# Optimization experiments

Hardware: AMD Instinct MI355X
Metric: run time of the kernel (lower is better)

The kernel has to match this reference:

```python
import jax, jax.numpy as jnp
from jax import lax
import numpy as np

L = 4
KH, KW = 3, 3


def setup_inputs() -> dict:
    key = jax.random.key(0)
    k1, k2, k3, k4 = jax.random.split(key, 4)
    B, H, W, C = 32, 512, 512, 3
    inputs = jax.random.normal(k1, (B, H, W, C), dtype=jnp.float32)
    # posterior_loc ~ 'random_normal' initializer (stddev 0.05 in keras)
    posterior_loc = 0.05 * jax.random.normal(k2, (KH, KW, C, 1), dtype=jnp.float32)
    # posterior_scale initialized to constant -5.0 (small perturbation for non-degeneracy)
    posterior_scale = jnp.full((KH, KW, C, 1), -5.0, dtype=jnp.float32) + 0.1 * jax.random.normal(k3, (KH, KW, C, 1), dtype=jnp.float32)
    # reparameterization noise, one independent sample per pyramid level
    eps = jax.random.normal(k4, (L, KH, KW, C, 1), dtype=jnp.float32)
    return {"inputs": inputs, "posterior_loc": posterior_loc, "posterior_scale": posterior_scale, "eps": eps}


def _center_mask(dtype):
    # zero at the kernel center, one elsewhere (scatter of sampled values into non-center taps)
    m = np.ones((KH, KW, 1, 1), dtype=np.float32)
    m[KH // 2, KW // 2, 0, 0] = 0.0
    return jnp.asarray(m, dtype=dtype)


def _depthwise(x, kernel_hwc1):
    # x: [B,h,w,C], kernel_hwc1: [KH,KW,C,1] (TF depthwise layout) -> HWIO [KH,KW,1,C]
    C = x.shape[-1]
    k = jnp.transpose(kernel_hwc1, (0, 1, 3, 2))
    return lax.conv_general_dilated(
        x, k, window_strides=(1, 1), padding="SAME",
        dimension_numbers=("NHWC", "HWIO", "NHWC"), feature_group_count=C)


def reference(inputs, posterior_loc, posterior_scale, eps):
    B, H, W, C = inputs.shape
    sigma = jax.nn.softplus(posterior_scale)  # posterior stddev
    mask = _center_mask(inputs.dtype)
    total_error = jnp.zeros((B, H, W), dtype=inputs.dtype)
    for l in range(1, L + 1):
        factor = 2 ** (l - 1)
        th, tw = H // factor, W // factor
        ds = jax.image.resize(inputs, (B, th, tw, C), method="bilinear", antialias=True)
        # sampled Bayesian kernel: center tap zeroed, then normalized per channel
        v = posterior_loc + sigma * eps[l - 1]
        kern = v * mask
        kern = kern / (jnp.sum(kern, axis=(0, 1), keepdims=True) + 1e-7)
        r_hat = _depthwise(ds, kern)
        err = ds - r_hat
        up = jax.image.resize(err, (B, H, W, C), method="bilinear", antialias=False)
        total_error = total_error + jnp.sum(up, axis=-1)
    recon = jnp.mean(jnp.sum(jnp.square(total_error), axis=(1, 2)))
    # KL(N(mu, sigma) || N(0,1)), summed; added once per conv call -> L times
    kl = jnp.sum(-jnp.log(sigma) + 0.5 * (jnp.square(sigma) + jnp.square(posterior_loc)) - 0.5)
    return recon + L * kl
```

## Files before the change

kernel.cpp:

```cpp
#include <hip/hip_runtime.h>
#include <hip/hip_fp16.h>
#include <math.h>

#define BB 32
#define HH 512
#define WW 512
#define CC 3
#define LL 4

typedef _Float16 h2_t __attribute__((ext_vector_type(2)));

static __device__ __forceinline__ float softplusf_(float x) {
    if (x > 20.f) return x;
    return log1pf(expf(x));
}
static __device__ __forceinline__ int iclamp_(int v, int lo, int hi) {
    return v < lo ? lo : (v > hi ? hi : v);
}

__global__ void prep_kernel(const float* __restrict__ loc, const float* __restrict__ scale,
                            const float* __restrict__ eps, float* __restrict__ knorm,
                            double* __restrict__ kl_out) {
    int tid = threadIdx.x;
    float klv = 0.f;
    if (tid < 27) {
        float s = softplusf_(scale[tid]);
        float m = loc[tid];
        klv = -logf(s) + 0.5f * (s * s + m * m) - 0.5f;
    }
    #pragma unroll
    for (int off = 32; off; off >>= 1) klv += __shfl_down(klv, off);
    if (tid == 0) *kl_out = (double)klv;
    if (tid < 12) {
        int l = tid / 3;
        int c = tid - l * 3;
        float v[9];
        float sum = 0.f;
        #pragma unroll
        for (int t = 0; t < 9; ++t) {
            int idx = t * 3 + c;
            float s = softplusf_(scale[idx]);
            float val = loc[idx] + s * eps[l * 27 + idx];
            if (t == 4) val = 0.f;
            v[t] = val;
            sum += val;
        }
        float denom = sum + 1e-7f;
        #pragma unroll
        for (int t = 0; t < 9; ++t)
            knorm[l * 27 + t * 3 + c] = v[t] / denom;
    }
}

#define PSH 544
#define RESC 1.1428571428571428f

__global__ void hpass_kernel(const float* __restrict__ x, __half* __restrict__ xh2,
                             __half* __restrict__ xh4, __half* __restrict__ xh8) {
    __shared__ __align__(16) __half planes[4 * 3 * PSH];
    const int tid = threadIdx.x;
    const int lane = tid & 63;
    const int wv = tid >> 6;
    const int bh = blockIdx.x * 4 + wv;
    __half* pl = planes + wv * (3 * PSH);

    const float4* src = (const float4*)(x + bh * (WW * CC));
    #pragma unroll
    for (int s = 0; s < 6; ++s) {
        int i = lane + (s << 6);
        float4 v = src[i];
        int g = i << 2;
        int j = g / 3;
        int c = g - j * 3;
        float e[4] = {v.x, v.y, v.z, v.w};
        #pragma unroll
        for (int u = 0; u < 4; ++u) {
            pl[c * PSH + 17 + j] = __float2half_rn(e[u]);
            ++c;
            if (c == 3) { c = 0; ++j; }
        }
    }
    {
        int t = lane;
        if (t < 96) {
            int pp = t >> 5, k = t & 31;
            int hi = (k < 17) ? k : (512 + k);
            pl[pp * PSH + hi] = __float2half_rn(0.f);
        }
        t = lane + 64;
        if (t < 96) {
            int pp = t >> 5, k = t & 31;
            int hi = (k < 17) ? k : (512 + k);
            pl[pp * PSH + hi] = __float2half_rn(0.f);
        }
    }
    asm volatile("s_waitcnt lgkmcnt(0)" ::: "memory");

    if (xh2) {
        const h2_t P0 = {(_Float16)0.125f, (_Float16)0.375f};
        const h2_t P1 = {(_Float16)0.375f, (_Float16)0.125f};
        __half* o2 = xh2 + bh * 768;
        #pragma unroll
        for (int s = 0; s < 4; ++s) {
            int ow = lane + (s << 6);
            float res[3];
            #pragma unroll
            for (int c = 0; c < 3; ++c) {
                const __half* p = pl + c * PSH;
                int hb2 = 2 * lane + 128 * s + 16;
                h2_t v0 = *(const h2_t*)&p[hb2];
                h2_t v1 = *(const h2_t*)&p[hb2 + 2];
                float a = __builtin_amdgcn_fdot2(v0, P0, 0.f, false);
                a = __builtin_amdgcn_fdot2(v1, P1, a, false);
                res[c] = a;
            }
            if (s == 0 && lane == 0) { res[0] *= RESC; res[1] *= RESC; res[2] *= RESC; }
            if (s == 3 && lane == 63) { res[0] *= RESC; res[1] *= RESC; res[2] *= RESC; }
            o2[ow * 3 + 0] = __float2half_rn(res[0]);
            o2[ow * 3 + 1] = __float2half_rn(res[1]);
            o2[ow * 3 + 2] = __float2half_rn(res[2]);
        }
    }
    if (xh4) {
        const h2_t P0 = {(_Float16)0.f,      (_Float16)0.03125f};
        const h2_t P1 = {(_Float16)0.09375f, (_Float16)0.15625f};
        const h2_t P2 = {(_Float16)0.21875f, (_Float16)0.21875f};
        const h2_t P3 = {(_Float16)0.15625f, (_Float16)0.09375f};
        const h2_t P4 = {(_Float16)0.03125f, (_Float16)0.f};
        __half* o4 = xh4 + bh * 384;
        #pragma unroll
        for (int s = 0; s < 2; ++s) {
            int ow = lane + (s << 6);
            float res[3];
            #pragma unroll
            for (int c = 0; c < 3; ++c) {
                const __half* p = pl + c * PSH;
                int hb2 = 4 * lane + 256 * s + 14;
                float a = __builtin_amdgcn_fdot2(*(const h2_t*)&p[hb2], P0, 0.f, false);
                a = __builtin_amdgcn_fdot2(*(const h2_t*)&p[hb2 + 2], P1, a, false);
                a = __builtin_amdgcn_fdot2(*(const h2_t*)&p[hb2 + 4], P2, a, false);
                a = __builtin_amdgcn_fdot2(*(const h2_t*)&p[hb2 + 6], P3, a, false);
                a = __builtin_amdgcn_fdot2(*(const h2_t*)&p[hb2 + 8], P4, a, false);
                res[c] = a;
            }
            if (s == 0 && lane == 0) { res[0] *= RESC; res[1] *= RESC; res[2] *= RESC; }
            if (s == 1 && lane == 63) { res[0] *= RESC; res[1] *= RESC; res[2] *= RESC; }
            o4[ow * 3 + 0] = __float2half_rn(res[0]);
            o4[ow * 3 + 1] = __float2half_rn(res[1]);
            o4[ow * 3 + 2] = __float2half_rn(res[2]);
        }
    }
    if (xh8) {
        const h2_t Q0 = {(_Float16)0.f,         (_Float16)0.0078125f};
        const h2_t Q1 = {(_Float16)0.0234375f,  (_Float16)0.0390625f};
        const h2_t Q2 = {(_Float16)0.0546875f,  (_Float16)0.0703125f};
        const h2_t Q3 = {(_Float16)0.0859375f,  (_Float16)0.1015625f};
        const h2_t Q4 = {(_Float16)0.1171875f,  (_Float16)0.1171875f};
        const h2_t Q5 = {(_Float16)0.1015625f,  (_Float16)0.0859375f};
        const h2_t Q6 = {(_Float16)0.0703125f,  (_Float16)0.0546875f};
        const h2_t Q7 = {(_Float16)0.0390625f,  (_Float16)0.0234375f};
        const h2_t Q8 = {(_Float16)0.0078125f,  (_Float16)0.f};
        __half* o8 = xh8 + bh * 192;
        int ow = lane;
        float res[3];
        #pragma unroll
        for (int c = 0; c < 3; ++c) {
            const __half* p = pl + c * PSH;
            int hb2 = 8 * lane + 12;
            float a = __builtin_amdgcn_fdot2(*(const h2_t*)&p[hb2], Q0, 0.f, false);
            a = __builtin_amdgcn_fdot2(*(const h2_t*)&p[hb2 + 2], Q1, a, false);
            a = __builtin_amdgcn_fdot2(*(const h2_t*)&p[hb2 + 4], Q2, a, false);
            a = __builtin_amdgcn_fdot2(*(const h2_t*)&p[hb2 + 6], Q3, a, false);
            a = __builtin_amdgcn_fdot2(*(const h2_t*)&p[hb2 + 8], Q4, a, false);
            a = __builtin_amdgcn_fdot2(*(const h2_t*)&p[hb2 + 10], Q5, a, false);
            a = __builtin_amdgcn_fdot2(*(const h2_t*)&p[hb2 + 12], Q6, a, false);
            a = __builtin_amdgcn_fdot2(*(const h2_t*)&p[hb2 + 14], Q7, a, false);
            a = __builtin_amdgcn_fdot2(*(const h2_t*)&p[hb2 + 16], Q8, a, false);
            res[c] = a;
        }
        if (lane == 0) { res[0] *= RESC; res[1] *= RESC; res[2] *= RESC; }
        if (lane == 63) { res[0] *= RESC; res[1] *= RESC; res[2] *= RESC; }
        o8[ow * 3 + 0] = __float2half_rn(res[0]);
        o8[ow * 3 + 1] = __float2half_rn(res[1]);
        o8[ow * 3 + 2] = __float2half_rn(res[2]);
    }
}

template <int F, int THB>
static __device__ __forceinline__ void level_body(const __half* __restrict__ xh,
                                                  const float* __restrict__ knorm_all, int lvl,
                                                  float* __restrict__ es, int bx, int by, int b,
                                                  char* smem_raw) {
    constexpr int TH = HH / F, TW = WW / F, TW3 = TW * 3, TAPS = 2 * F;
    constexpr int RS = (THB + 3) * F;
    constexpr int DR = THB + 2;
    __half* stg = (__half*)smem_raw;
    float* dst = (float*)(smem_raw + RS * 108 * 2);
    float* wvv = dst + DR * 108;
    float* kn = wvv + DR * TAPS;
    int owb = bx * 32, ohb = by * THB;
    int tid = threadIdx.x;
    if (tid < 27) kn[tid] = knorm_all[lvl * 27 + tid];
    if (tid >= 32 && tid < 32 + DR) {
        int r = tid - 32;
        int oh = ohb - 1 + r;
        if (oh < 0 || oh >= TH) {
            #pragma unroll
            for (int k = 0; k < TAPS; ++k) wvv[r * TAPS + k] = 0.f;
        } else {
            float sfh = (oh + 0.5f) * F - 0.5f;
            int j0 = oh * F - F / 2;
            float tmp[TAPS]; float s = 0.f;
            #pragma unroll
            for (int k = 0; k < TAPS; ++k) {
                int j = j0 + k;
                float w = (j >= 0 && j < HH) ? (1.f - fabsf(j - sfh) * (1.0f / F)) : 0.f;
                tmp[k] = w; s += w;
            }
            float inv = 1.f / s;
            #pragma unroll
            for (int k = 0; k < TAPS; ++k) wvv[r * TAPS + k] = tmp[k] * inv;
        }
    }
    int jmin = (ohb - 1) * F - F / 2;
    int cb = owb * 3 - 4;
    bool fast = (cb >= 0) && (cb + 108 <= TW3);
    const __half* xb = xh + b * (HH * TW3);
    for (int i = tid; i < RS * 27; i += 256) {
        int r = i / 27;
        int c4 = (i - r * 27) * 4;
        int jh = iclamp_(jmin + r, 0, HH - 1);
        const __half* rp = xb + jh * TW3;
        if (fast) {
            *(ushort4*)&stg[r * 108 + c4] = *(const ushort4*)(rp + cb + c4);
        } else {
            #pragma unroll
            for (int u = 0; u < 4; ++u) {
                int col = iclamp_(cb + c4 + u, 0, TW3 - 1);
                stg[r * 108 + c4 + u] = rp[col];
            }
        }
    }
    __syncthreads();
    for (int i = tid; i < DR * 27; i += 256) {
        int r = i / 27;
        int c4 = (i - r * 27) * 4;
        int gc = cb + c4;
        float v0 = 0, v1 = 0, v2 = 0, v3 = 0;
        if ((unsigned)gc < (unsigned)TW3) {
            const __half* sp = &stg[r * F * 108 + c4];
            const float* wr = &wvv[r * TAPS];
            #pragma unroll
            for (int k = 0; k < TAPS; ++k) {
                float wk = wr[k];
                const __half2* h2 = (const __half2*)(sp + k * 108);
                float2 f0 = __half22float2(h2[0]);
                float2 f1 = __half22float2(h2[1]);
                v0 += wk * f0.x; v1 += wk * f0.y;
                v2 += wk * f1.x; v3 += wk * f1.y;
            }
        }
        float4 q; q.x = v0; q.y = v1; q.z = v2; q.w = v3;
        *(float4*)&dst[r * 108 + c4] = q;
    }
    __syncthreads();
    for (int i = tid; i < THB * 32; i += 256) {
        int wl = i & 31, hl = i >> 5;
        int base = hl * 108 + wl * 3 + 1;
        float e = 0.f;
        #pragma unroll
        for (int c = 0; c < 3; ++c) {
            float conv = 0.f;
            #pragma unroll
            for (int dh = 0; dh < 3; ++dh)
                #pragma unroll
                for (int dw = 0; dw < 3; ++dw)
                    conv += kn[(dh * 3 + dw) * 3 + c] * dst[base + dh * 108 + dw * 3 + c];
            e += dst[base + 108 + 3 + c] - conv;
        }
        es[b * (TH * TW) + (ohb + hl) * TW + owb + wl] = e;
    }
}

__global__ void levels_kernel(const __half* __restrict__ xh2, const __half* __restrict__ xh4,
                              const __half* __restrict__ xh8, const float* __restrict__ knorm,
                              float* __restrict__ es2, float* __restrict__ es3,
                              float* __restrict__ es4, int block_base) {
    __shared__ __align__(16) char smem[16896];
    int vb = blockIdx.x + block_base;
    if (vb < 4096) {
        level_body<2, 16>(xh2, knorm, 1, es2, vb & 7, (vb >> 3) & 15, vb >> 7, smem);
    } else if (vb < 6144) {
        int l = vb - 4096;
        level_body<4, 8>(xh4, knorm, 2, es3, l & 3, (l >> 2) & 15, l >> 6, smem);
    } else {
        int l = vb - 6144;
        level_body<8, 4>(xh8, knorm, 3, es4, l & 1, (l >> 1) & 15, l >> 5, smem);
    }
}

#define FPS 35
#define FPC (34 * FPS)
__global__ void __launch_bounds__(256, 8)
fused_kernel(const float* __restrict__ x, const float* __restrict__ knorm,
             const float* __restrict__ es2, const float* __restrict__ es3,
             const float* __restrict__ es4, double* __restrict__ partials) {
    __shared__ __align__(16) float planes[3 * FPC];
    __shared__ float e2t[18 * 19];
    __shared__ float e3t[10 * 11];
    __shared__ float e4t[6 * 7];
    __shared__ float kn[27];
    __shared__ float smf[4];
    int b = blockIdx.z;
    int hb = blockIdx.y * 32, wb = blockIdx.x * 32;
    int tid = threadIdx.x;
    if (tid < 27) kn[tid] = knorm[tid];
    const float* xb = x + b * (HH * WW * CC);
    int cb = wb * 3 - 4;
    bool fastc = (cb >= 0) && (cb + 108 <= WW * CC);
    for (int i = tid; i < 918; i += 256) {
        int r = i / 27;
        int f0 = (i - r * 27) * 4;
        int gh = hb - 1 + r;
        bool ghv = (unsigned)gh < (unsigned)HH;
        float vv[4] = {0.f, 0.f, 0.f, 0.f};
        if (ghv) {
            const float* rp = xb + gh * (WW * CC);
            if (fastc) {
                float4 v = *(const float4*)(rp + cb + f0);
                vv[0] = v.x; vv[1] = v.y; vv[2] = v.z; vv[3] = v.w;
            } else {
                int g0 = cb + f0;
                #pragma unroll
                for (int u = 0; u < 4; ++u)
                    vv[u] = ((unsigned)(g0 + u) < (unsigned)(WW * CC)) ? rp[g0 + u] : 0.f;
            }
        }
        #pragma unroll
        for (int u = 0; u < 4; ++u) {
            int f = f0 + u;
            if (f >= 1 && f <= 102) {
                int lc = (f - 1) / 3;
                int ch = (f - 1) - lc * 3;
                planes[ch * FPC + r * FPS + lc] = vv[u];
            }
        }
    }
    {
        const float* e2b = es2 + b * (256 * 256);
        int h0 = hb / 2 - 1, w0 = wb / 2 - 1;
        for (int i = tid; i < 18 * 32; i += 256) {
            int r = i >> 5, c = i & 31;
            if (c < 18) {
                int gh = iclamp_(h0 + r, 0, 255);
                int gw = iclamp_(w0 + c, 0, 255);
                e2t[r * 19 + c] = e2b[gh * 256 + gw];
            }
        }
        const float* e3b = es3 + b * (128 * 128);
        int h03 = hb / 4 - 1, w03 = wb / 4 - 1;
        if (tid < 160) {
            int r = tid >> 4, c = tid & 15;
            if (c < 10) {
                int gh = iclamp_(h03 + r, 0, 127);
                int gw = iclamp_(w03 + c, 0, 127);
                e3t[r * 11 + c] = e3b[gh * 128 + gw];
            }
        }
        const float* e4b = es4 + b * (64 * 64);
        int h04 = hb / 8 - 1, w04 = wb / 8 - 1;
        if (tid < 48) {
            int r = tid >> 3, c = tid & 7;
            if (c < 6) {
                int gh = iclamp_(h04 + r, 0, 63);
                int gw = iclamp_(w04 + c, 0, 63);
                e4t[r * 7 + c] = e4b[gh * 64 + gw];
            }
        }
    }
    __syncthreads();

    int q = tid >> 3;
    int a = tid & 7;
    float cv0 = 0, cv1 = 0, cv2 = 0, cv3 = 0;
    float ce0 = 0, ce1 = 0, ce2 = 0, ce3 = 0;
    #pragma unroll
    for (int c = 0; c < 3; ++c) {
        const float* P = planes + c * FPC;
        #pragma unroll
        for (int dh = 0; dh < 3; ++dh) {
            const float* r0 = P + (q + dh) * FPS + 4 * a;
            float w0 = r0[0], w1 = r0[1], w2 = r0[2], w3 = r0[3], w4 = r0[4], w5 = r0[5];
            float ka = kn[dh * 9 + c], kb = kn[dh * 9 + 3 + c], kc = kn[dh * 9 + 6 + c];
            cv0 += ka * w0 + kb * w1 + kc * w2;
            cv1 += ka * w1 + kb * w2 + kc * w3;
            cv2 += ka * w2 + kb * w3 + kc * w4;
            cv3 += ka * w3 + kb * w4 + kc * w5;
            if (dh == 1) { ce0 += w1; ce1 += w2; ce2 += w3; ce3 += w4; }
        }
    }
    float e[4] = {ce0 - cv0, ce1 - cv1, ce2 - cv2, ce3 - cv3};

    int n2 = q & 1;   float fh2 = n2 ? 0.25f : 0.75f;               int rh2 = (q >> 1) + n2;
    int n4 = q & 3;   float fh4 = ((n4 + 2) & 3) * 0.25f + 0.125f;  int rh4 = (q >> 2) + (n4 < 2 ? 0 : 1);
    int n8 = q & 7;   float fh8 = ((n8 + 4) & 7) * 0.125f + 0.0625f; int rh8 = (q >> 3) + (n8 < 4 ? 0 : 1);
    {
        const float* r0 = &e2t[rh2 * 19 + 2 * a];
        const float* r1 = r0 + 19;
        float t0 = r0[0], t1 = r0[1], t2 = r0[2], t3 = r0[3];
        float b0 = r1[0], b1 = r1[1], b2 = r1[2], b3 = r1[3];
        float top, bot;
        top = t0 + 0.75f * (t1 - t0); bot = b0 + 0.75f * (b1 - b0); e[0] += top + fh2 * (bot - top);
        top = t1 + 0.25f * (t2 - t1); bot = b1 + 0.25f * (b2 - b1); e[1] += top + fh2 * (bot - top);
        top = t1 + 0.75f * (t2 - t1); bot = b1 + 0.75f * (b2 - b1); e[2] += top + fh2 * (bot - top);
        top = t2 + 0.25f * (t3 - t2); bot = b2 + 0.25f * (b3 - b2); e[3] += top + fh2 * (bot - top);
    }
    {
        const float* r0 = &e3t[rh4 * 11 + a];
        const float* r1 = r0 + 11;
        float t0 = r0[0], t1 = r0[1], t2 = r0[2];
        float b0 = r1[0], b1 = r1[1], b2 = r1[2];
        float top, bot;
        top = t0 + 0.625f * (t1 - t0); bot = b0 + 0.625f * (b1 - b0); e[0] += top + fh4 * (bot - top);
        top = t0 + 0.875f * (t1 - t0); bot = b0 + 0.875f * (b1 - b0); e[1] += top + fh4 * (bot - top);
        top = t1 + 0.125f * (t2 - t1); bot = b1 + 0.125f * (b2 - b1); e[2] += top + fh4 * (bot - top);
        top = t1 + 0.375f * (t2 - t1); bot = b1 + 0.375f * (b2 - b1); e[3] += top + fh4 * (bot - top);
    }
    {
        int rw8 = (a >> 1) + (a & 1);
        const float* r0 = &e4t[rh8 * 7 + rw8];
        const float* r1 = r0 + 7;
        float t0 = r0[0], t1 = r0[1];
        float b0 = r1[0], b1 = r1[1];
        float fwb = (a & 1) ? 0.0625f : 0.5625f;
        #pragma unroll
        for (int p = 0; p < 4; ++p) {
            float fw = fwb + 0.125f * p;
            float top = t0 + fw * (t1 - t0);
            float bot = b0 + fw * (b1 - b0);
            e[p] += top + fh8 * (bot - top);
        }
    }
    float acc = e[0] * e[0] + e[1] * e[1] + e[2] * e[2] + e[3] * e[3];
    #pragma unroll
    for (int off = 32; off; off >>= 1) acc += __shfl_down(acc, off);
    if ((tid & 63) == 0) smf[tid >> 6] = acc;
    __syncthreads();
    if (tid == 0) {
        double s = (double)smf[0] + (double)smf[1] + (double)smf[2] + (double)smf[3];
        partials[(b * 16 + blockIdx.y) * 16 + blockIdx.x] = s;
    }
}

__global__ void final_kernel(const double* __restrict__ partials, int n,
                             const double* __restrict__ kl, float* __restrict__ out) {
    __shared__ double sm[1024];
    double acc = 0.0;
    for (int i = threadIdx.x; i < n; i += 1024) acc += partials[i];
    sm[threadIdx.x] = acc;
    __syncthreads();
    for (int s = 512; s > 0; s >>= 1) {
        if (threadIdx.x < (unsigned)s) sm[threadIdx.x] += sm[threadIdx.x + s];
        __syncthreads();
    }
    if (threadIdx.x == 0) out[0] = (float)(sm[0] / (double)BB + (double)LL * kl[0]);
}

extern "C" void kernel_launch(void* const* d_in, const int* in_sizes, int n_in,
                              void* d_out, int out_size, void* d_ws, size_t ws_size,
                              hipStream_t stream) {
    const float* x = (const float*)d_in[0];
    const float* loc = (const float*)d_in[1];
    const float* scale = (const float*)d_in[2];
    const float* eps = (const float*)d_in[3];
    float* out = (float*)d_out;

    char* ws = (char*)d_ws;
    float* knorm = (float*)(ws + 0);
    double* kl = (double*)(ws + 512);
    double* partials = (double*)(ws + 1024);
    float* es4 = (float*)(ws + 131072);
    float* es3 = (float*)(ws + 655360);
    float* es2 = (float*)(ws + 2752512);
    (void)in_sizes; (void)n_in; (void)out_size;

    prep_kernel<<<1, 64, 0, stream>>>(loc, scale, eps, knorm, kl);

    const size_t SINGLE_NEED = 55181312ull;
    if (ws_size >= SINGLE_NEED) {
        __half* xh2 = (__half*)(ws + 11141120);
        __half* xh4 = (__half*)(ws + 36306944);
        __half* xh8 = (__half*)(ws + 48889856);
        hpass_kernel<<<BB * HH / 4, 256, 0, stream>>>(x, xh2, xh4, xh8);
        levels_kernel<<<7168, 256, 0, stream>>>(xh2, xh4, xh8, knorm, es2, es3, es4, 0);
    } else {
        __half* xh4 = (__half*)(ws + 11141120);
        __half* xh8 = (__half*)(ws + 23724032);
        __half* xh2 = (__half*)(ws + 11141120);
        hpass_kernel<<<BB * HH / 4, 256, 0, stream>>>(x, nullptr, xh4, xh8);
        levels_kernel<<<3072, 256, 0, stream>>>(nullptr, xh4, xh8, knorm, es2, es3, es4, 4096);
        hpass_kernel<<<BB * HH / 4, 256, 0, stream>>>(x, xh2, nullptr, nullptr);
        levels_kernel<<<4096, 256, 0, stream>>>(xh2, nullptr, nullptr, knorm, es2, es3, es4, 0);
    }

    fused_kernel<<<dim3(16, 16, BB), 256, 0, stream>>>(x, knorm, es2, es3, es4, partials);
    final_kernel<<<1, 1024, 0, stream>>>(partials, 8192, kl, out);
}
```

Before: 106.1 us.

## Keep interleaved channel layout in shared tile and use vectorized LDS reads

The fused kernel's input tile is now stored in shared memory in its original interleaved NHWC order, written as float4, instead of being scattered into three per-channel planes. The stencil reads 20 floats per row with five float4 loads and skips the zero centre tap explicitly. The aim is to cut the scalar scatter stores and per-element index math during staging and the many scalar LDS reads in the compute loop. In exchange it uses more registers per thread, lowers the launch-bounds occupancy hint from 8 to 6, and the strided float4 LDS reads may cause bank conflicts.

```diff
diff --git a/kernel.cpp b/kernel.cpp
--- a/kernel.cpp
+++ b/kernel.cpp
@@ -299,13 +299,12 @@
     }
 }
 
-#define FPS 35
-#define FPC (34 * FPS)
-__global__ void __launch_bounds__(256, 8)
+#define FXS 116
+__global__ void __launch_bounds__(256, 6)
 fused_kernel(const float* __restrict__ x, const float* __restrict__ knorm,
              const float* __restrict__ es2, const float* __restrict__ es3,
              const float* __restrict__ es4, double* __restrict__ partials) {
-    __shared__ __align__(16) float planes[3 * FPC];
+    __shared__ __align__(16) float xt[34 * FXS];
     __shared__ float e2t[18 * 19];
     __shared__ float e3t[10 * 11];
     __shared__ float e4t[6 * 7];
@@ -316,35 +315,29 @@
     int tid = threadIdx.x;
     if (tid < 27) kn[tid] = knorm[tid];
     const float* xb = x + b * (HH * WW * CC);
-    int cb = wb * 3 - 4;
-    bool fastc = (cb >= 0) && (cb + 108 <= WW * CC);
-    for (int i = tid; i < 918; i += 256) {
-        int r = i / 27;
-        int f0 = (i - r * 27) * 4;
+    const int cb2 = wb * 3 - 4;
+    for (int i = tid; i < 34 * 29; i += 256) {
+        int r = i / 29;
+        int k = i - r * 29;
         int gh = hb - 1 + r;
         bool ghv = (unsigned)gh < (unsigned)HH;
-        float vv[4] = {0.f, 0.f, 0.f, 0.f};
+        int g0 = cb2 + 4 * k;
+        float4 v = {0.f, 0.f, 0.f, 0.f};
         if (ghv) {
             const float* rp = xb + gh * (WW * CC);
-            if (fastc) {
-                float4 v = *(const float4*)(rp + cb + f0);
-                vv[0] = v.x; vv[1] = v.y; vv[2] = v.z; vv[3] = v.w;
+            if (g0 >= 0 && g0 + 4 <= WW * CC) {
+                v = *(const float4*)(rp + g0);
             } else {
-                int g0 = cb + f0;
+                float vv[4];
                 #pragma unroll
-                for (int u = 0; u < 4; ++u)
-                    vv[u] = ((unsigned)(g0 + u) < (unsigned)(WW * CC)) ? rp[g0 + u] : 0.f;
-            }
-        }
-        #pragma unroll
-        for (int u = 0; u < 4; ++u) {
-            int f = f0 + u;
-            if (f >= 1 && f <= 102) {
-                int lc = (f - 1) / 3;
-                int ch = (f - 1) - lc * 3;
-                planes[ch * FPC + r * FPS + lc] = vv[u];
-            }
-        }
+                for (int u = 0; u < 4; ++u) {
+                    int g = g0 + u;
+                    vv[u] = ((unsigned)g < (unsigned)(WW * CC)) ? rp[g] : 0.f;
+                }
+                v.x = vv[0]; v.y = vv[1]; v.z = vv[2]; v.w = vv[3];
+            }
+        }
+        *(float4*)&xt[r * FXS + 4 * k] = v;
     }
     {
         const float* e2b = es2 + b * (256 * 256);
@@ -385,18 +378,31 @@
     float cv0 = 0, cv1 = 0, cv2 = 0, cv3 = 0;
     float ce0 = 0, ce1 = 0, ce2 = 0, ce3 = 0;
     #pragma unroll
-    for (int c = 0; c < 3; ++c) {
-        const float* P = planes + c * FPC;
-        #pragma unroll
-        for (int dh = 0; dh < 3; ++dh) {
-            const float* r0 = P + (q + dh) * FPS + 4 * a;
-            float w0 = r0[0], w1 = r0[1], w2 = r0[2], w3 = r0[3], w4 = r0[4], w5 = r0[5];
-            float ka = kn[dh * 9 + c], kb = kn[dh * 9 + 3 + c], kc = kn[dh * 9 + 6 + c];
-            cv0 += ka * w0 + kb * w1 + kc * w2;
-            cv1 += ka * w1 + kb * w2 + kc * w3;
-            cv2 += ka * w2 + kb * w3 + kc * w4;
-            cv3 += ka * w3 + kb * w4 + kc * w5;
-            if (dh == 1) { ce0 += w1; ce1 += w2; ce2 += w3; ce3 += w4; }
+    for (int dh = 0; dh < 3; ++dh) {
+        const float* rp = &xt[(q + dh) * FXS + 12 * a];
+        float w[20];
+        #pragma unroll
+        for (int j = 0; j < 5; ++j) {
+            float4 t = *(const float4*)(rp + 4 * j);
+            w[4 * j + 0] = t.x; w[4 * j + 1] = t.y; w[4 * j + 2] = t.z; w[4 * j + 3] = t.w;
+        }
+        #pragma unroll
+        for (int dw = 0; dw < 3; ++dw) {
+            #pragma unroll
+            for (int c = 0; c < 3; ++c) {
+                if (dh == 1 && dw == 1) continue;
+                float k = kn[(dh * 3 + dw) * 3 + c];
+                cv0 += k * w[3 * 0 + 3 * dw + c + 1];
+                cv1 += k * w[3 * 1 + 3 * dw + c + 1];
+                cv2 += k * w[3 * 2 + 3 * dw + c + 1];
+                cv3 += k * w[3 * 3 + 3 * dw + c + 1];
+            }
+        }
+        if (dh == 1) {
+            ce0 += w[4] + w[5] + w[6];
+            ce1 += w[7] + w[8] + w[9];
+            ce2 += w[10] + w[11] + w[12];
+            ce3 += w[13] + w[14] + w[15];
         }
     }
     float e[4] = {ce0 - cv0, ce1 - cv1, ce2 - cv2, ce3 - cv3};
```

Result: slower. 114.8 us (+8.2%).
